# Performance work log

Hardware: AMD Instinct MI355X
Metric: run time of the kernel (lower is better)

## Reference

```python
import jax, jax.numpy as jnp
import numpy as np

DIM = 1024
H = 16
HEAD_DIM = 64
HIDDEN = H * HEAD_DIM  # == DIM, required by the module's reshape
SCALE = HEAD_DIM ** -0.5


def setup_inputs() -> dict:
    key = jax.random.key(0)
    k_x, k_qkv, k_w1, k_b1 = jax.random.split(key, 4)
    B, N = 8, 1024
    x = jax.random.normal(k_x, (B, N, DIM), dtype=jnp.float32)
    # nn.Linear stores weight as [out, in]; we keep [in, out] for x @ W
    w_qkv = jax.random.normal(k_qkv, (DIM, 3 * HIDDEN), dtype=jnp.float32) * (DIM ** -0.5)
    w_out = jax.random.normal(k_w1, (HIDDEN, DIM), dtype=jnp.float32) * (HIDDEN ** -0.5)
    b_out = jax.random.normal(k_b1, (DIM,), dtype=jnp.float32) * 0.02
    return {"x": x, "w_qkv": w_qkv, "w_out": w_out, "b_out": b_out}


def reference(x, w_qkv, w_out, b_out):
    B, N, C = x.shape
    # QKV projection (no bias), split into heads
    qkv = (x @ w_qkv).reshape(B, N, 3, H, C // H)
    q, k, v = qkv[:, :, 0], qkv[:, :, 1], qkv[:, :, 2]  # [B, N, H, d]
    attn = jnp.einsum("bqhd,bkhd->bhqk", q, k) * SCALE
    attn = jax.nn.softmax(attn, axis=-1)  # dropout inactive at eval
    out = jnp.einsum("bhqk,bkhd->bqhd", attn, v).reshape(B, N, C)
    return out @ w_out + b_out
```

## Files before the change

kernel.cpp:

```cpp
#include <hip/hip_runtime.h>
#include <hip/hip_bf16.h>

#define B_SZ 8
#define SEQ 1024
#define DIM_ 1024
#define NH 16
#define HD 64
#define M_TOT (B_SZ*SEQ)
#define N_QKV (3*DIM_)

typedef __attribute__((ext_vector_type(8))) short bf16x8;
typedef __attribute__((ext_vector_type(4))) float f32x4;

typedef const __attribute__((address_space(1))) void gvoid;
typedef __attribute__((address_space(3))) void lvoid;

__device__ __forceinline__ short f2bf(float f){
  union { __hip_bfloat16 h; short s; } u;
  u.h = __float2bfloat16(f);
  return u.s;
}

__global__ void cvt_kernel(const float* __restrict__ in, short* __restrict__ out, int n4){
  int i = blockIdx.x*blockDim.x + threadIdx.x;
  int stride = gridDim.x*blockDim.x;
  for (; i < n4; i += stride){
    float4 v = reinterpret_cast<const float4*>(in)[i];
    short4 s;
    s.x = f2bf(v.x); s.y = f2bf(v.y); s.z = f2bf(v.z); s.w = f2bf(v.w);
    reinterpret_cast<short4*>(out)[i] = s;
  }
}

__global__ void tconv_kernel(const float* __restrict__ in, short* __restrict__ out, int R, int C){
  __shared__ alignas(16) short tile[64][66];
  const int l = threadIdx.x & 63, w = threadIdx.x >> 6;
  const int r0 = blockIdx.y * 64, c0 = blockIdx.x * 64;
  #pragma unroll
  for (int rr = 0; rr < 16; ++rr){
    int r = w + rr*4;
    tile[r][l] = f2bf(in[(size_t)(r0+r)*C + c0 + l]);
  }
  __syncthreads();
  #pragma unroll
  for (int cc = 0; cc < 16; ++cc){
    int c = w + cc*4;
    out[(size_t)(c0+c)*R + r0 + l] = tile[l][c];
  }
}

template<int EPI, int GX>
__global__ __launch_bounds__(256, 4) void gemm5(
    const short* __restrict__ A, const short* __restrict__ Bt,
    int M, int Nn, int K,
    short* __restrict__ Qb, short* __restrict__ Kb, short* __restrict__ Vtb,
    const float* __restrict__ bias, float* __restrict__ outF)
{
  __shared__ alignas(16) short As[2][128*32];
  __shared__ alignas(16) short Bs[2][128*32];

  const int orig = blockIdx.x;
  const int xcd = orig & 7, t = orig >> 3;
  const int by = xcd*8 + t/GX, bx = t % GX;

  const int tid = threadIdx.x;
  const int l = tid & 63, wid = tid >> 6;
  const int wr = wid >> 1, wc = wid & 1;
  const int lr = l & 15, lw = l >> 4;
  const int sw = (lr >> 1) & 3;
  const int m0 = by * 128, n0 = bx * 128;

  f32x4 acc[4][4];
  const f32x4 zz = {0.f,0.f,0.f,0.f};
  #pragma unroll
  for (int m=0;m<4;m++)
    #pragma unroll
    for (int n=0;n<4;n++) acc[m][n] = zz;

  auto STAGE = [&](int buf, int kt){
    const int k0 = kt << 5;
    #pragma unroll
    for (int j=0;j<2;j++){
      const int idx = j*256 + tid;
      const int row = idx >> 2;
      const int ws  = (idx & 3) ^ ((row >> 1) & 3);
      __builtin_amdgcn_global_load_lds(
          (gvoid*)(A + (size_t)(m0+row)*K + k0 + ws*8),
          (lvoid*)(&As[buf][idx*8]), 16, 0, 0);
    }
    #pragma unroll
    for (int j=0;j<2;j++){
      const int idx = j*256 + tid;
      const int row = idx >> 2;
      const int ws  = (idx & 3) ^ ((row >> 1) & 3);
      __builtin_amdgcn_global_load_lds(
          (gvoid*)(Bt + (size_t)(n0+row)*K + k0 + ws*8),
          (lvoid*)(&Bs[buf][idx*8]), 16, 0, 0);
    }
  };

  STAGE(0, 0);
  __syncthreads();

  const int NT = K >> 5;
  int buf = 0;
  for (int kt = 0; kt < NT; ++kt){
    if (kt + 1 < NT) STAGE(buf ^ 1, kt + 1);

    bf16x8 af[4], bfr[4];
    const int wsel = (lw ^ sw) << 3;
    #pragma unroll
    for (int m=0;m<4;m++){
      const int r = wr*64 + m*16 + lr;
      af[m] = *(const bf16x8*)(&As[buf][r*32 + wsel]);
    }
    #pragma unroll
    for (int n=0;n<4;n++){
      const int r = wc*64 + n*16 + lr;
      bfr[n] = *(const bf16x8*)(&Bs[buf][r*32 + wsel]);
    }
    __builtin_amdgcn_s_setprio(1);
    #pragma unroll
    for (int m=0;m<4;m++)
      #pragma unroll
      for (int n=0;n<4;n++)
        acc[m][n] = __builtin_amdgcn_mfma_f32_16x16x32_bf16(af[m], bfr[n], acc[m][n], 0, 0, 0);
    __builtin_amdgcn_s_setprio(0);

    __syncthreads();
    buf ^= 1;
  }

  #pragma unroll
  for (int n=0;n<4;n++){
    const int col = n0 + wc*64 + n*16 + lr;
    float bv = 0.f;
    if (EPI == 1) bv = bias[col];
    #pragma unroll
    for (int m=0;m<4;m++){
      const int rbase = m0 + wr*64 + m*16 + (lw<<2);
      #pragma unroll
      for (int ri=0;ri<4;ri++){
        const int row = rbase + ri;
        const float v = acc[m][n][ri];
        if (EPI == 0){
          const int three = col >> 10;
          const int cc = col & 1023;
          const int h = cc >> 6, d = cc & 63;
          const int b = row >> 10, nn = row & 1023;
          const int bh = b*NH + h;
          if (three == 0)      Qb[((size_t)bh*SEQ + nn)*HD + d] = f2bf(v * 0.1803368801f);
          else if (three == 1) Kb[((size_t)bh*SEQ + nn)*HD + d] = f2bf(v);
          else                 Vtb[((size_t)bh*HD + d)*SEQ + nn] = f2bf(v);
        } else {
          outF[(size_t)row*Nn + col] = v + bv;
        }
      }
    }
  }
}

__global__ __launch_bounds__(256) void attn_kernel(
    const short* __restrict__ Q, const short* __restrict__ Kb,
    const short* __restrict__ Vt, short* __restrict__ Ao)
{
  __shared__ alignas(16) short Ks[2][64*64];
  __shared__ alignas(16) short Vs[2][64*64];
  __shared__ alignas(16) short Ps[4][16*72];

  const int tid = threadIdx.x;
  const int l = tid & 63, w = tid >> 6;
  const int bid = blockIdx.x;
  const int qt = bid & 15, bh = bid >> 4;
  const int b = bh >> 4, h = bh & 15;
  const size_t base = (size_t)bh << 16;

  const int lr = l & 15;
  const int q4 = l >> 4;
  const int lk = q4 << 3;
  const int sw8 = lr & 7;

  const int qrow = qt*64 + w*16 + lr;
  const short* qp = Q + base + (size_t)qrow*HD + lk;
  const bf16x8 qf0 = *(const bf16x8*)qp;
  const bf16x8 qf1 = *(const bf16x8*)(qp + 32);

  float m_run = -1e30f, l_run = 0.f;
  f32x4 o[4];
  #pragma unroll
  for (int i=0;i<4;i++) o[i] = f32x4{0.f,0.f,0.f,0.f};

  bf16x8 kr[2], vr[2];
  auto load_tile = [&](int kt){
    const int kv0 = kt*64;
    #pragma unroll
    for (int p=0;p<2;p++){
      const int idx = tid + p*256;
      const int row = idx >> 3, c8 = (idx & 7) << 3;
      kr[p] = *(const bf16x8*)(Kb + base + (size_t)(kv0+row)*HD + c8);
      vr[p] = *(const bf16x8*)(Vt + base + (size_t)row*SEQ + kv0 + c8);
    }
  };
  auto write_tile = [&](int bi){
    #pragma unroll
    for (int p=0;p<2;p++){
      const int idx = tid + p*256;
      const int row = idx >> 3;
      const int wsw = ((idx & 7) ^ (row & 7)) << 3;
      *(bf16x8*)(&Ks[bi][row*64 + wsw]) = kr[p];
      *(bf16x8*)(&Vs[bi][row*64 + wsw]) = vr[p];
    }
  };

  load_tile(0);
  write_tile(0);
  __syncthreads();

  int cur = 0;
  for (int kt = 0; kt < 16; ++kt){
    if (kt < 15) load_tile(kt+1);

    const short* kb = &Ks[cur][0];
    const short* vb = &Vs[cur][0];

    f32x4 s[4];
    #pragma unroll
    for (int cg=0;cg<4;cg++) s[cg] = f32x4{0.f,0.f,0.f,0.f};
    __builtin_amdgcn_s_setprio(1);
    #pragma unroll
    for (int cg=0;cg<4;cg++){
      const short* kp = kb + (cg*16 + lr)*64;
      bf16x8 kf0 = *(const bf16x8*)(kp + ((q4     ^ sw8) << 3));
      bf16x8 kf1 = *(const bf16x8*)(kp + (((q4+4) ^ sw8) << 3));
      s[cg] = __builtin_amdgcn_mfma_f32_16x16x32_bf16(kf0, qf0, s[cg], 0,0,0);
      s[cg] = __builtin_amdgcn_mfma_f32_16x16x32_bf16(kf1, qf1, s[cg], 0,0,0);
    }
    __builtin_amdgcn_s_setprio(0);

    float mt = s[0][0];
    #pragma unroll
    for (int cg=0;cg<4;cg++)
      #pragma unroll
      for (int ri=0;ri<4;ri++) mt = fmaxf(mt, s[cg][ri]);
    mt = fmaxf(mt, __shfl_xor(mt, 16));
    mt = fmaxf(mt, __shfl_xor(mt, 32));

    const float mn = fmaxf(m_run, mt);
    const float corr = __builtin_amdgcn_exp2f(m_run - mn);
    m_run = mn;

    float p[4][4], rs = 0.f;
    #pragma unroll
    for (int cg=0;cg<4;cg++)
      #pragma unroll
      for (int ri=0;ri<4;ri++){
        p[cg][ri] = __builtin_amdgcn_exp2f(s[cg][ri] - mn);
        rs += p[cg][ri];
      }
    rs += __shfl_xor(rs, 16);
    rs += __shfl_xor(rs, 32);
    l_run = l_run*corr + rs;

    short* pw = &Ps[w][0];
    #pragma unroll
    for (int cg=0;cg<4;cg++){
      short4 pk;
      pk.x = f2bf(p[cg][0]); pk.y = f2bf(p[cg][1]);
      pk.z = f2bf(p[cg][2]); pk.w = f2bf(p[cg][3]);
      *(short4*)(pw + lr*72 + cg*16 + q4*4) = pk;
    }

    float corr_r[4];
    #pragma unroll
    for (int ri=0;ri<4;ri++) corr_r[ri] = __shfl(corr, (q4<<2) + ri);
    #pragma unroll
    for (int dg=0;dg<4;dg++)
      #pragma unroll
      for (int ri=0;ri<4;ri++) o[dg][ri] *= corr_r[ri];

    const bf16x8 pa0 = *(const bf16x8*)(pw + lr*72 + lk);
    const bf16x8 pa1 = *(const bf16x8*)(pw + lr*72 + lk + 32);
    __builtin_amdgcn_s_setprio(1);
    #pragma unroll
    for (int dg=0;dg<4;dg++){
      const short* vp = vb + (dg*16 + lr)*64;
      bf16x8 vf0 = *(const bf16x8*)(vp + ((q4     ^ sw8) << 3));
      bf16x8 vf1 = *(const bf16x8*)(vp + (((q4+4) ^ sw8) << 3));
      o[dg] = __builtin_amdgcn_mfma_f32_16x16x32_bf16(pa0, vf0, o[dg], 0,0,0);
      o[dg] = __builtin_amdgcn_mfma_f32_16x16x32_bf16(pa1, vf1, o[dg], 0,0,0);
    }
    __builtin_amdgcn_s_setprio(0);

    if (kt < 15) write_tile(cur ^ 1);
    __syncthreads();
    cur ^= 1;
  }

  float linv[4];
  #pragma unroll
  for (int ri=0;ri<4;ri++) linv[ri] = 1.0f / __shfl(l_run, (q4<<2) + ri);
  #pragma unroll
  for (int ri=0;ri<4;ri++){
    const int row = qt*64 + w*16 + (q4<<2) + ri;
    short* op = Ao + ((size_t)(b*SEQ + row))*DIM_ + h*HD;
    #pragma unroll
    for (int dg=0;dg<4;dg++)
      op[dg*16 + lr] = f2bf(o[dg][ri] * linv[ri]);
  }
}

extern "C" void kernel_launch(void* const* d_in, const int* in_sizes, int n_in,
                              void* d_out, int out_size, void* d_ws, size_t ws_size,
                              hipStream_t stream)
{
  (void)in_sizes; (void)n_in; (void)out_size; (void)ws_size;
  const float* x     = (const float*)d_in[0];
  const float* w_qkv = (const float*)d_in[1];
  const float* w_out = (const float*)d_in[2];
  const float* b_out = (const float*)d_in[3];
  float* out = (float*)d_out;

  char* ws = (char*)d_ws;
  const size_t MB = (size_t)1 << 20;
  short* xb    = (short*)(ws);
  short* wqkvT = (short*)(ws + 16*MB);
  short* woutT = (short*)(ws + 22*MB);
  short* Qb    = (short*)(ws + 24*MB);
  short* Kb    = (short*)(ws + 40*MB);
  short* Vtb   = (short*)(ws + 56*MB);
  short* Aob   = (short*)(ws + 72*MB);

  cvt_kernel<<<2048, 256, 0, stream>>>(x, xb, (M_TOT*DIM_)/4);
  tconv_kernel<<<dim3(N_QKV/64, DIM_/64), 256, 0, stream>>>(w_qkv, wqkvT, DIM_, N_QKV);
  tconv_kernel<<<dim3(DIM_/64, DIM_/64), 256, 0, stream>>>(w_out, woutT, DIM_, DIM_);

  gemm5<0,24><<<1536, 256, 0, stream>>>(
      xb, wqkvT, M_TOT, N_QKV, DIM_, Qb, Kb, Vtb, nullptr, nullptr);

  attn_kernel<<<B_SZ*NH*(SEQ/64), 256, 0, stream>>>(Qb, Kb, Vtb, Aob);

  gemm5<1,8><<<512, 256, 0, stream>>>(
      Aob, woutT, M_TOT, DIM_, DIM_, nullptr, nullptr, nullptr, b_out, out);
}
```

Baseline: 208.8 us.

## Split QKV GEMM into QK and V launches, vectorize V-transpose stores

```diff
diff --git a/kernel.cpp b/kernel.cpp
--- a/kernel.cpp
+++ b/kernel.cpp
@@ -49,7 +49,7 @@
   }
 }
 
-template<int EPI, int GX>
+template<int EPI, int GX, int NOFF>
 __global__ __launch_bounds__(256, 4) void gemm5(
     const short* __restrict__ A, const short* __restrict__ Bt,
     int M, int Nn, int K,
@@ -68,7 +68,7 @@
   const int wr = wid >> 1, wc = wid & 1;
   const int lr = l & 15, lw = l >> 4;
   const int sw = (lr >> 1) & 3;
-  const int m0 = by * 128, n0 = bx * 128;
+  const int m0 = by * 128, n0 = (bx + NOFF) * 128;
 
   f32x4 acc[4][4];
   const f32x4 zz = {0.f,0.f,0.f,0.f};
@@ -119,13 +119,11 @@
       const int r = wc*64 + n*16 + lr;
       bfr[n] = *(const bf16x8*)(&Bs[buf][r*32 + wsel]);
     }
-    __builtin_amdgcn_s_setprio(1);
     #pragma unroll
     for (int m=0;m<4;m++)
       #pragma unroll
       for (int n=0;n<4;n++)
         acc[m][n] = __builtin_amdgcn_mfma_f32_16x16x32_bf16(af[m], bfr[n], acc[m][n], 0, 0, 0);
-    __builtin_amdgcn_s_setprio(0);
 
     __syncthreads();
     buf ^= 1;
@@ -134,27 +132,38 @@
   #pragma unroll
   for (int n=0;n<4;n++){
     const int col = n0 + wc*64 + n*16 + lr;
-    float bv = 0.f;
-    if (EPI == 1) bv = bias[col];
-    #pragma unroll
-    for (int m=0;m<4;m++){
-      const int rbase = m0 + wr*64 + m*16 + (lw<<2);
-      #pragma unroll
-      for (int ri=0;ri<4;ri++){
-        const int row = rbase + ri;
-        const float v = acc[m][n][ri];
-        if (EPI == 0){
-          const int three = col >> 10;
-          const int cc = col & 1023;
-          const int h = cc >> 6, d = cc & 63;
-          const int b = row >> 10, nn = row & 1023;
-          const int bh = b*NH + h;
-          if (three == 0)      Qb[((size_t)bh*SEQ + nn)*HD + d] = f2bf(v * 0.1803368801f);
-          else if (three == 1) Kb[((size_t)bh*SEQ + nn)*HD + d] = f2bf(v);
-          else                 Vtb[((size_t)bh*HD + d)*SEQ + nn] = f2bf(v);
+    if (EPI == 0){
+      const int three = col >> 10;
+      const int cc = col & 1023;
+      const int h = cc >> 6, d = cc & 63;
+      #pragma unroll
+      for (int m=0;m<4;m++){
+        const int rbase = m0 + wr*64 + m*16 + (lw<<2);
+        const int b = rbase >> 10, nn = rbase & 1023;
+        const int bh = b*NH + h;
+        if (three == 2){
+          short4 pk;
+          pk.x = f2bf(acc[m][n][0]); pk.y = f2bf(acc[m][n][1]);
+          pk.z = f2bf(acc[m][n][2]); pk.w = f2bf(acc[m][n][3]);
+          *(short4*)(&Vtb[((size_t)bh*HD + d)*SEQ + nn]) = pk;
+        } else if (three == 0){
+          #pragma unroll
+          for (int ri=0;ri<4;ri++)
+            Qb[((size_t)bh*SEQ + nn + ri)*HD + d] = f2bf(acc[m][n][ri] * 0.1803368801f);
         } else {
-          outF[(size_t)row*Nn + col] = v + bv;
+          #pragma unroll
+          for (int ri=0;ri<4;ri++)
+            Kb[((size_t)bh*SEQ + nn + ri)*HD + d] = f2bf(acc[m][n][ri]);
         }
+      }
+    } else {
+      const float bv = bias[col];
+      #pragma unroll
+      for (int m=0;m<4;m++){
+        const int rbase = m0 + wr*64 + m*16 + (lw<<2);
+        #pragma unroll
+        for (int ri=0;ri<4;ri++)
+          outF[(size_t)(rbase+ri)*Nn + col] = acc[m][n][ri] + bv;
       }
     }
   }
@@ -334,11 +343,14 @@
   tconv_kernel<<<dim3(N_QKV/64, DIM_/64), 256, 0, stream>>>(w_qkv, wqkvT, DIM_, N_QKV);
   tconv_kernel<<<dim3(DIM_/64, DIM_/64), 256, 0, stream>>>(w_out, woutT, DIM_, DIM_);
 
-  gemm5<0,24><<<1536, 256, 0, stream>>>(
+  gemm5<0,16,0><<<1024, 256, 0, stream>>>(
       xb, wqkvT, M_TOT, N_QKV, DIM_, Qb, Kb, Vtb, nullptr, nullptr);
 
+  gemm5<0,8,16><<<512, 256, 0, stream>>>(
+      xb, wqkvT, M_TOT, N_QKV, DIM_, Qb, Kb, Vtb, nullptr, nullptr);
+
   attn_kernel<<<B_SZ*NH*(SEQ/64), 256, 0, stream>>>(Qb, Kb, Vtb, Aob);
 
-  gemm5<1,8><<<512, 256, 0, stream>>>(
+  gemm5<1,8,0><<<512, 256, 0, stream>>>(
       Aob, woutT, M_TOT, DIM_, DIM_, nullptr, nullptr, nullptr, b_out, out);
 }
```

After: 191.1 us. -8.5%, faster.
